# Optimization experiments

Measured on AMD Instinct MI355X. Metric: run time of the kernel, lower is better.

The kernel has to match this reference:

```python
import jax, jax.numpy as jnp
import numpy as np

B, S, HID = 2, 2048, 2048
NH, NKV = 16, 4
HD = HID // NH  # 128
GROUPS = NH // NKV


def _rope(x, cos, sin):
    # x: [B, S, H, D]; cos/sin: [S, D//2]
    xr = x.reshape(*x.shape[:-1], HD // 2, 2)
    x0, x1 = xr[..., 0], xr[..., 1]
    c = cos[None, :, None, :]
    s = sin[None, :, None, :]
    o0 = x0 * c - x1 * s
    o1 = x0 * s + x1 * c
    return jnp.stack([o0, o1], axis=-1).reshape(*x.shape)


def setup_inputs() -> dict:
    key = jax.random.key(0)
    k1, k2, k3, k4, k5, k6 = jax.random.split(key, 6)
    hidden_states = jax.random.normal(k1, (B, S, HID), dtype=jnp.float32)
    # RoPE frequencies (llama-style)
    inv_freq = 1.0 / (10000.0 ** (np.arange(0, HD, 2, dtype=np.float32) / HD))
    t = np.arange(S, dtype=np.float32)
    ang = np.outer(t, inv_freq)  # [S, HD//2]
    freqs_cos = jnp.asarray(np.cos(ang), dtype=jnp.float32)
    freqs_sin = jnp.asarray(np.sin(ang), dtype=jnp.float32)
    # additive causal mask [1,1,S,S]
    causal = jnp.triu(jnp.full((S, S), -1e9, dtype=jnp.float32), k=1)
    attention_mask = causal[None, None]
    sc = 0.02
    Wq = jax.random.normal(k2, (NH * HD, HID), dtype=jnp.float32) * sc
    Wk = jax.random.normal(k3, (NKV * HD, HID), dtype=jnp.float32) * sc
    Wv = jax.random.normal(k4, (NKV * HD, HID), dtype=jnp.float32) * sc
    Wo = jax.random.normal(k5, (HID, NH * HD), dtype=jnp.float32) * sc
    return {"hidden_states": hidden_states, "freqs_cos": freqs_cos,
            "freqs_sin": freqs_sin, "attention_mask": attention_mask,
            "Wq": Wq, "Wk": Wk, "Wv": Wv, "Wo": Wo}


def reference(hidden_states, freqs_cos, freqs_sin, attention_mask, Wq, Wk, Wv, Wo):
    xq = (hidden_states @ Wq.T).reshape(B, S, NH, HD)
    xk = (hidden_states @ Wk.T).reshape(B, S, NKV, HD)
    xv = (hidden_states @ Wv.T).reshape(B, S, NKV, HD)
    xq = _rope(xq, freqs_cos, freqs_sin)
    xk = _rope(xk, freqs_cos, freqs_sin)
    # expand KV heads for GQA: [B,S,NKV,D] -> [B,S,NH,D]
    xk = jnp.repeat(xk, GROUPS, axis=2)
    xv = jnp.repeat(xv, GROUPS, axis=2)
    q = xq.transpose(0, 2, 1, 3)  # [B,H,S,D]
    k = xk.transpose(0, 2, 1, 3)
    v = xv.transpose(0, 2, 1, 3)
    scores = jnp.einsum('bhqd,bhkd->bhqk', q, k) / jnp.sqrt(jnp.float32(HD))
    scores = scores + attention_mask
    probs = jax.nn.softmax(scores, axis=-1)
    out = jnp.einsum('bhqk,bhkd->bhqd', probs, v)
    out = out.transpose(0, 2, 1, 3).reshape(B, S, NH * HD)
    return out @ Wo.T
```

## Files before the change

### kernel.cpp

```cpp
#include <hip/hip_runtime.h>


typedef __attribute__((ext_vector_type(8))) short bf16x8;
typedef __attribute__((ext_vector_type(4))) float f32x4;
typedef __attribute__((ext_vector_type(16))) float f32x16;
typedef __attribute__((ext_vector_type(4))) unsigned short u16x4;
typedef unsigned short u16;

#define B_   2
#define S_   2048
#define HID_ 2048
#define NH_  16
#define NKV_ 4
#define HD_  128

__device__ __forceinline__ u16 f2bf(float f) {
  unsigned u = __float_as_uint(f);
  u = (u + 0x7FFFu + ((u >> 16) & 1u)) >> 16;
  return (u16)u;
}
__device__ __forceinline__ float bf2f(u16 h) {
  return __uint_as_float(((unsigned)h) << 16);
}

__device__ __forceinline__ void gl_lds16(const void* g, void* l) {
  __builtin_amdgcn_global_load_lds(
      (const __attribute__((address_space(1))) void*)g,
      (__attribute__((address_space(3))) void*)l, 16, 0, 0);
}

__global__ void convert_bf16(const float* __restrict__ src, u16* __restrict__ dst, int n8) {
  int i = blockIdx.x * 256 + threadIdx.x;
  if (i >= n8) return;
  const float4* s = (const float4*)src + (size_t)i * 2;
  float4 a = s[0], b = s[1];
  union { u16 u[8]; uint4 v; } o;
  o.u[0] = f2bf(a.x); o.u[1] = f2bf(a.y); o.u[2] = f2bf(a.z); o.u[3] = f2bf(a.w);
  o.u[4] = f2bf(b.x); o.u[5] = f2bf(b.y); o.u[6] = f2bf(b.z); o.u[7] = f2bf(b.w);
  ((uint4*)dst)[i] = o.v;
}

template<int EPI>
__launch_bounds__(256, 2)
__global__ void gemm128(const u16* __restrict__ A, const u16* __restrict__ Bm,
                        float* __restrict__ C, u16* __restrict__ Qb,
                        u16* __restrict__ Kb, u16* __restrict__ Vb,
                        int N, int K)
{
  __shared__ u16 As[128 * 64];
  __shared__ u16 Bs[128 * 64];
  const int tid = threadIdx.x;
  const int lane = tid & 63;
  const int w = tid >> 6;
  const int lo = lane & 15, hi = lane >> 4;
  const int wr = w >> 1, wc = w & 1;
  const int rowA0 = blockIdx.x * 128;
  const int rowB0 = blockIdx.y * 128;

  f32x4 acc[4][4] = {};

  for (int kt = 0; kt < K; kt += 64) {
    __syncthreads();
#pragma unroll
    for (int it = 0; it < 4; ++it) {
      int c = it * 256 + tid;
      int r = c >> 3;
      int cb = (c & 7) * 8;
      gl_lds16(A + (size_t)(rowA0 + r) * K + kt + cb, (char*)As + c * 16);
      gl_lds16(Bm + (size_t)(rowB0 + r) * K + kt + cb, (char*)Bs + c * 16);
    }
    __syncthreads();
#pragma unroll
    for (int kk = 0; kk < 64; kk += 32) {
      bf16x8 af[4], bfr[4];
#pragma unroll
      for (int m = 0; m < 4; ++m)
        af[m] = *(const bf16x8*)(As + (wr * 64 + m * 16 + lo) * 64 + kk + hi * 8);
#pragma unroll
      for (int n = 0; n < 4; ++n)
        bfr[n] = *(const bf16x8*)(Bs + (wc * 64 + n * 16 + lo) * 64 + kk + hi * 8);
#pragma unroll
      for (int m = 0; m < 4; ++m)
#pragma unroll
        for (int n = 0; n < 4; ++n)
          acc[m][n] = __builtin_amdgcn_mfma_f32_16x16x32_bf16(af[m], bfr[n], acc[m][n], 0, 0, 0);
    }
  }

#pragma unroll
  for (int m = 0; m < 4; ++m) {
#pragma unroll
    for (int n = 0; n < 4; ++n) {
#pragma unroll
      for (int r = 0; r < 4; ++r) {
        int grow = rowA0 + wr * 64 + m * 16 + hi * 4 + r;
        int gcol = rowB0 + wc * 64 + n * 16 + lo;
        float v = acc[m][n][r];
        if (EPI == 0) {
          C[(size_t)grow * N + gcol] = v;
        } else {
          int bb = grow >> 11, s = grow & 2047;
          u16 hv = f2bf(v);
          if (gcol < 2048) {
            int h = gcol >> 7, d = gcol & 127;
            Qb[(((size_t)bb * NH_ + h) * S_ + s) * HD_ + d] = hv;
          } else if (gcol < 2560) {
            int h = (gcol - 2048) >> 7, d = gcol & 127;
            Kb[(((size_t)bb * NKV_ + h) * S_ + s) * HD_ + d] = hv;
          } else {
            int h = (gcol - 2560) >> 7, d = gcol & 127;
            Vb[(((size_t)bb * NKV_ + h) * S_ + s) * HD_ + d] = hv;
          }
        }
      }
    }
  }
}

__global__ void rope_k(u16* __restrict__ Qb, u16* __restrict__ Kb,
                       const float* __restrict__ fcos, const float* __restrict__ fsin)
{
  int idx = blockIdx.x * 256 + threadIdx.x;
  int chunk = idx & 15;
  int s = (idx >> 4) & 2047;
  int hs = idx >> 15;
  u16* p = (hs < 32) ? (Qb + ((size_t)hs * S_ + s) * HD_ + chunk * 8)
                     : (Kb + ((size_t)(hs - 32) * S_ + s) * HD_ + chunk * 8);
  uint4 raw = *(uint4*)p;
  float4 c4 = *(const float4*)(fcos + (size_t)s * 64 + chunk * 4);
  float4 s4 = *(const float4*)(fsin + (size_t)s * 64 + chunk * 4);
  float cc[4] = {c4.x, c4.y, c4.z, c4.w};
  float ss[4] = {s4.x, s4.y, s4.z, s4.w};
  unsigned* rw = (unsigned*)&raw;
#pragma unroll
  for (int j = 0; j < 4; ++j) {
    float x0 = bf2f((u16)(rw[j] & 0xFFFFu));
    float x1 = bf2f((u16)(rw[j] >> 16));
    float o0 = x0 * cc[j] - x1 * ss[j];
    float o1 = x0 * ss[j] + x1 * cc[j];
    rw[j] = (unsigned)f2bf(o0) | ((unsigned)f2bf(o1) << 16);
  }
  *(uint4*)p = raw;
}

__global__ void transpose_v(const u16* __restrict__ Vb, u16* __restrict__ Vtg)
{
  __shared__ u16 t[64][65];
  const int st = blockIdx.x, dt = blockIdx.y, hs = blockIdx.z;
  const u16* src = Vb + ((size_t)hs * S_ + st * 64) * HD_ + dt * 64;
#pragma unroll
  for (int it = 0; it < 2; ++it) {
    int c = it * 256 + threadIdx.x;
    int r = c >> 3, cb = (c & 7) * 8;
    uint4 v = *(const uint4*)(src + (size_t)r * HD_ + cb);
    u16* u = (u16*)&v;
#pragma unroll
    for (int e = 0; e < 8; ++e) t[r][cb + e] = u[e];
  }
  __syncthreads();
#pragma unroll
  for (int it = 0; it < 2; ++it) {
    int c = it * 256 + threadIdx.x;
    int r2 = c >> 3, cb2 = (c & 7) * 8;
    union { u16 u[8]; uint4 v; } o;
#pragma unroll
    for (int e = 0; e < 8; ++e) o.u[e] = t[cb2 + e][r2];
    *(uint4*)(Vtg + ((size_t)hs * HD_ + dt * 64 + r2) * S_ + st * 64 + cb2) = o.v;
  }
}

__launch_bounds__(256, 2)
__global__ void flash_attn(const u16* __restrict__ Qb, const u16* __restrict__ Kb,
                           const u16* __restrict__ Vtg, u16* __restrict__ AO)
{
  const int tid = threadIdx.x, lane = tid & 63, w = tid >> 6;
  const int ql = lane & 31, hh = lane >> 5;
  const int x = blockIdx.x, h = blockIdx.y, b = blockIdx.z, kvh = h >> 2;
  const u16* Qh = Qb + ((size_t)b * NH_ + h) * S_ * HD_;
  const u16* Kh = Kb + ((size_t)b * NKV_ + kvh) * S_ * HD_;
  const u16* Vh = Vtg + ((size_t)b * NKV_ + kvh) * HD_ * S_;
  const float cf = 0.12752704581383682f;
  const float NEG = -30000.f;

  const int qt = (w == 0) ? x : (w == 1) ? (63 - x) : (w == 2) ? (31 - x) : (32 + x);
  const int q0 = qt * 32;
  const int qg = q0 + ql;
  const int nt = (qt >> 1) + 1;

  bf16x8 qf[8];
#pragma unroll
  for (int s = 0; s < 8; ++s)
    qf[s] = *(const bf16x8*)(Qh + (size_t)qg * HD_ + s * 16 + hh * 8);

  f32x16 o[4] = {};
  float m = NEG, l = 0.f;

  for (int t = 0; t < nt; ++t) {
    const int kt = t * 64;
    const u16* Kt = Kh + (size_t)kt * HD_;

    bf16x8 k0[8], k1[8];
#pragma unroll
    for (int sl = 0; sl < 8; ++sl)
      k0[sl] = *(const bf16x8*)(Kt + (size_t)ql * HD_ + sl * 16 + hh * 8);
#pragma unroll
    for (int sl = 0; sl < 8; ++sl)
      k1[sl] = *(const bf16x8*)(Kt + (size_t)(32 + ql) * HD_ + sl * 16 + hh * 8);
    f32x16 st[2] = {};
    __builtin_amdgcn_s_setprio(1);
#pragma unroll
    for (int sl = 0; sl < 8; ++sl) {
      st[0] = __builtin_amdgcn_mfma_f32_32x32x16_bf16(k0[sl], qf[sl], st[0], 0, 0, 0);
      st[1] = __builtin_amdgcn_mfma_f32_32x32x16_bf16(k1[sl], qf[sl], st[1], 0, 0, 0);
    }
    __builtin_amdgcn_s_setprio(0);

    if (kt + 63 > q0) {
#pragma unroll
      for (int i = 0; i < 2; ++i)
#pragma unroll
        for (int r = 0; r < 16; ++r) {
          int kv = kt + 32 * i + (r & 3) + 8 * (r >> 2) + 4 * hh;
          if (kv > qg) st[i][r] = NEG;
        }
    }

    float mx[8];
#pragma unroll
    for (int r = 0; r < 8; ++r)
      mx[r] = fmaxf(fmaxf(st[0][r], st[0][r + 8]), fmaxf(st[1][r], st[1][r + 8]));
#pragma unroll
    for (int d = 4; d > 0; d >>= 1)
#pragma unroll
      for (int r = 0; r < d; ++r) mx[r] = fmaxf(mx[r], mx[r + d]);
    float tmax = fmaxf(mx[0], __shfl_xor(mx[0], 32));

    if (!__all((tmax - m) * cf <= 8.f)) {
      float mn = fmaxf(m, tmax);
      float rs = __builtin_exp2f((m - mn) * cf);
      m = mn; l *= rs;
#pragma unroll
      for (int dt = 0; dt < 4; ++dt)
#pragma unroll
        for (int r = 0; r < 16; ++r) o[dt][r] *= rs;
    }

    const float mc = m * cf;
#pragma unroll
    for (int i = 0; i < 2; ++i)
#pragma unroll
      for (int r = 0; r < 16; ++r)
        st[i][r] = __builtin_exp2f(__builtin_fmaf(st[i][r], cf, -mc));
    float sm[8];
#pragma unroll
    for (int r = 0; r < 8; ++r)
      sm[r] = (st[0][r] + st[0][r + 8]) + (st[1][r] + st[1][r + 8]);
#pragma unroll
    for (int d = 4; d > 0; d >>= 1)
#pragma unroll
      for (int r = 0; r < d; ++r) sm[r] += sm[r + d];
    l += sm[0] + __shfl_xor(sm[0], 32);

    bf16x8 pb[4];
#pragma unroll
    for (int i = 0; i < 2; ++i)
#pragma unroll
      for (int s = 0; s < 2; ++s) {
        unsigned wA, wC, wB, wD;
        asm("v_cvt_pk_bf16_f32 %0, %1, %2" : "=v"(wA) : "v"(st[i][8*s+0]), "v"(st[i][8*s+1]));
        asm("v_cvt_pk_bf16_f32 %0, %1, %2" : "=v"(wC) : "v"(st[i][8*s+2]), "v"(st[i][8*s+3]));
        asm("v_cvt_pk_bf16_f32 %0, %1, %2" : "=v"(wB) : "v"(st[i][8*s+4]), "v"(st[i][8*s+5]));
        asm("v_cvt_pk_bf16_f32 %0, %1, %2" : "=v"(wD) : "v"(st[i][8*s+6]), "v"(st[i][8*s+7]));
        unsigned tA = (unsigned)__shfl_xor((int)wA, 32);
        unsigned tB = (unsigned)__shfl_xor((int)wB, 32);
        unsigned tC = (unsigned)__shfl_xor((int)wC, 32);
        unsigned tD = (unsigned)__shfl_xor((int)wD, 32);
        union { unsigned u[4]; bf16x8 v; } pk;
        pk.u[0] = hh ? tB : wA;
        pk.u[1] = hh ? tD : wC;
        pk.u[2] = hh ? wB : tA;
        pk.u[3] = hh ? wD : tC;
        pb[2 * i + s] = pk.v;
      }

#pragma unroll
    for (int dt = 0; dt < 4; ++dt) {
      bf16x8 vf[4];
#pragma unroll
      for (int ks = 0; ks < 4; ++ks)
        vf[ks] = *(const bf16x8*)(Vh + (size_t)(32 * dt + ql) * S_ + kt + ks * 16 + hh * 8);
      __builtin_amdgcn_s_setprio(1);
#pragma unroll
      for (int ks = 0; ks < 4; ++ks)
        o[dt] = __builtin_amdgcn_mfma_f32_32x32x16_bf16(vf[ks], pb[ks], o[dt], 0, 0, 0);
      __builtin_amdgcn_s_setprio(0);
    }
  }

  const float inv = 1.f / l;
#pragma unroll
  for (int dt = 0; dt < 4; ++dt)
#pragma unroll
    for (int g = 0; g < 4; ++g) {
      u16x4 pk4;
#pragma unroll
      for (int e = 0; e < 4; ++e) pk4[e] = f2bf(o[dt][4 * g + e] * inv);
      *(u16x4*)(AO + ((size_t)b * S_ + qg) * HID_ + h * HD_ + 32 * dt + 8 * g + 4 * hh) = pk4;
    }
}

extern "C" void kernel_launch(void* const* d_in, const int* in_sizes, int n_in,
                              void* d_out, int out_size, void* d_ws, size_t ws_size,
                              hipStream_t stream)
{
  (void)in_sizes; (void)n_in; (void)out_size; (void)ws_size;
  const float* X  = (const float*)d_in[0];
  const float* fc = (const float*)d_in[1];
  const float* fs = (const float*)d_in[2];
  const float* Wq = (const float*)d_in[4];
  const float* Wk = (const float*)d_in[5];
  const float* Wv = (const float*)d_in[6];
  const float* Wo = (const float*)d_in[7];
  float* out = (float*)d_out;

  u16* Xb  = (u16*)d_ws;
  u16* Wb  = Xb + (size_t)4096 * 2048;
  u16* Qb  = Wb + (size_t)3072 * 2048;
  u16* Kb  = Qb + (size_t)B_ * NH_ * S_ * HD_;
  u16* Vb  = Kb + (size_t)B_ * NKV_ * S_ * HD_;
  u16* AO  = Xb;
  u16* Wob = Wb;
  u16* Vtg = Wb + (size_t)2048 * 2048;

  convert_bf16<<<4096, 256, 0, stream>>>(X,  Xb,               4096 * 2048 / 8);
  convert_bf16<<<2048, 256, 0, stream>>>(Wq, Wb,               2048 * 2048 / 8);
  convert_bf16<<<512,  256, 0, stream>>>(Wk, Wb + 2048 * 2048, 512 * 2048 / 8);
  convert_bf16<<<512,  256, 0, stream>>>(Wv, Wb + 2560 * 2048, 512 * 2048 / 8);

  gemm128<1><<<dim3(32, 24), 256, 0, stream>>>(Xb, Wb, nullptr, Qb, Kb, Vb, 3072, 2048);

  convert_bf16<<<2048, 256, 0, stream>>>(Wo, Wob, 2048 * 2048 / 8);

  transpose_v<<<dim3(32, 2, 8), 256, 0, stream>>>(Vb, Vtg);

  rope_k<<<5120, 256, 0, stream>>>(Qb, Kb, fc, fs);

  flash_attn<<<dim3(16, NH_, B_), 256, 0, stream>>>(Qb, Kb, Vtg, AO);

  gemm128<0><<<dim3(32, 16), 256, 0, stream>>>(AO, Wob, out, nullptr, nullptr, nullptr, 2048, 2048);
}
```

Before: 289.8 us.

## Double-buffer K tile loads and prefetch V fragments in flash attention loop

The attention inner loop now keeps two register buffers for K tiles and issues the next tile's K loads right after the current QK^T MFMAs, so global-memory latency overlaps with softmax and PV work. V fragments are split into two halves loaded earlier, before masking and the softmax, so they are in flight during that computation. This raises register pressure considerably (32 extra bf16x8 K registers plus 16 V registers), which may lower occupancy or cause spills.

```diff
diff --git a/kernel.cpp b/kernel.cpp
--- a/kernel.cpp
+++ b/kernel.cpp
@@ -195,25 +195,37 @@
   f32x16 o[4] = {};
   float m = NEG, l = 0.f;
 
-  for (int t = 0; t < nt; ++t) {
+  bf16x8 kA[16], kB[16];
+
+  auto loadK = [&](bf16x8 (&kd)[16], int t) {
+    const u16* Kt = Kh + (size_t)(t * 64) * HD_;
+#pragma unroll
+    for (int sl = 0; sl < 8; ++sl) {
+      kd[sl]     = *(const bf16x8*)(Kt + (size_t)ql * HD_ + sl * 16 + hh * 8);
+      kd[8 + sl] = *(const bf16x8*)(Kt + (size_t)(32 + ql) * HD_ + sl * 16 + hh * 8);
+    }
+  };
+
+  auto body = [&](bf16x8 (&kc)[16], bf16x8 (&kn)[16], int t) {
     const int kt = t * 64;
-    const u16* Kt = Kh + (size_t)kt * HD_;
-
-    bf16x8 k0[8], k1[8];
-#pragma unroll
-    for (int sl = 0; sl < 8; ++sl)
-      k0[sl] = *(const bf16x8*)(Kt + (size_t)ql * HD_ + sl * 16 + hh * 8);
-#pragma unroll
-    for (int sl = 0; sl < 8; ++sl)
-      k1[sl] = *(const bf16x8*)(Kt + (size_t)(32 + ql) * HD_ + sl * 16 + hh * 8);
+
     f32x16 st[2] = {};
     __builtin_amdgcn_s_setprio(1);
 #pragma unroll
     for (int sl = 0; sl < 8; ++sl) {
-      st[0] = __builtin_amdgcn_mfma_f32_32x32x16_bf16(k0[sl], qf[sl], st[0], 0, 0, 0);
-      st[1] = __builtin_amdgcn_mfma_f32_32x32x16_bf16(k1[sl], qf[sl], st[1], 0, 0, 0);
+      st[0] = __builtin_amdgcn_mfma_f32_32x32x16_bf16(kc[sl],     qf[sl], st[0], 0, 0, 0);
+      st[1] = __builtin_amdgcn_mfma_f32_32x32x16_bf16(kc[8 + sl], qf[sl], st[1], 0, 0, 0);
     }
     __builtin_amdgcn_s_setprio(0);
+
+    if (t + 1 < nt) loadK(kn, t + 1);
+
+    bf16x8 vf0[8];
+#pragma unroll
+    for (int dt = 0; dt < 2; ++dt)
+#pragma unroll
+      for (int ks = 0; ks < 4; ++ks)
+        vf0[4 * dt + ks] = *(const bf16x8*)(Vh + (size_t)(32 * dt + ql) * S_ + kt + ks * 16 + hh * 8);
 
     if (kt + 63 > q0) {
 #pragma unroll
@@ -283,18 +295,31 @@
         pb[2 * i + s] = pk.v;
       }
 
-#pragma unroll
-    for (int dt = 0; dt < 4; ++dt) {
-      bf16x8 vf[4];
+    bf16x8 vf1[8];
+#pragma unroll
+    for (int dt = 0; dt < 2; ++dt)
 #pragma unroll
       for (int ks = 0; ks < 4; ++ks)
-        vf[ks] = *(const bf16x8*)(Vh + (size_t)(32 * dt + ql) * S_ + kt + ks * 16 + hh * 8);
-      __builtin_amdgcn_s_setprio(1);
+        vf1[4 * dt + ks] = *(const bf16x8*)(Vh + (size_t)(64 + 32 * dt + ql) * S_ + kt + ks * 16 + hh * 8);
+
+    __builtin_amdgcn_s_setprio(1);
+#pragma unroll
+    for (int dt = 0; dt < 2; ++dt)
 #pragma unroll
       for (int ks = 0; ks < 4; ++ks)
-        o[dt] = __builtin_amdgcn_mfma_f32_32x32x16_bf16(vf[ks], pb[ks], o[dt], 0, 0, 0);
-      __builtin_amdgcn_s_setprio(0);
-    }
+        o[dt] = __builtin_amdgcn_mfma_f32_32x32x16_bf16(vf0[4 * dt + ks], pb[ks], o[dt], 0, 0, 0);
+#pragma unroll
+    for (int dt = 0; dt < 2; ++dt)
+#pragma unroll
+      for (int ks = 0; ks < 4; ++ks)
+        o[2 + dt] = __builtin_amdgcn_mfma_f32_32x32x16_bf16(vf1[4 * dt + ks], pb[ks], o[2 + dt], 0, 0, 0);
+    __builtin_amdgcn_s_setprio(0);
+  };
+
+  loadK(kA, 0);
+  for (int t = 0; t < nt; ++t) {
+    if (t & 1) body(kB, kA, t);
+    else       body(kA, kB, t);
   }
 
   const float inv = 1.f / l;
```

New measurement: 648.5 us. 124% more time.

## Rework flash attention to 16x16x32 MFMA tiles with LDS P-reshuffle

Applied to the files above, without the earlier changes.

The flash attention kernel now uses 16-row query tiles per wave with 16x16x32 bf16 MFMAs instead of 32-row tiles with 32x32x16. The P matrix goes through a small per-wave LDS buffer instead of cross-lane shuffles. The grid becomes 1024 blocks with a linearised index that groups blocks sharing a KV head for cache locality. Launch bounds rise to 4 blocks per SM for higher occupancy. In exchange, each K and V element is reloaded for twice as many query tiles, and LDS traffic is added for P.

```diff
diff --git a/kernel.cpp b/kernel.cpp
--- a/kernel.cpp
+++ b/kernel.cpp
@@ -3,7 +3,6 @@
 
 typedef __attribute__((ext_vector_type(8))) short bf16x8;
 typedef __attribute__((ext_vector_type(4))) float f32x4;
-typedef __attribute__((ext_vector_type(16))) float f32x16;
 typedef __attribute__((ext_vector_type(4))) unsigned short u16x4;
 typedef unsigned short u16;
 
@@ -169,144 +168,145 @@
   }
 }
 
-__launch_bounds__(256, 2)
+__launch_bounds__(256, 4)
 __global__ void flash_attn(const u16* __restrict__ Qb, const u16* __restrict__ Kb,
                            const u16* __restrict__ Vtg, u16* __restrict__ AO)
 {
+  __shared__ u16 Ps[4][16 * 72];
+
   const int tid = threadIdx.x, lane = tid & 63, w = tid >> 6;
-  const int ql = lane & 31, hh = lane >> 5;
-  const int x = blockIdx.x, h = blockIdx.y, b = blockIdx.z, kvh = h >> 2;
+  const int qi = lane & 15, lh = lane >> 4;
+  const int lin = blockIdx.x;
+  const int g = lin & 7, idx = lin >> 3;
+  const int b = g >> 2, kvh = g & 3;
+  const int h = kvh * 4 + (idx >> 5);
+  const int x = idx & 31;
+
   const u16* Qh = Qb + ((size_t)b * NH_ + h) * S_ * HD_;
   const u16* Kh = Kb + ((size_t)b * NKV_ + kvh) * S_ * HD_;
   const u16* Vh = Vtg + ((size_t)b * NKV_ + kvh) * HD_ * S_;
   const float cf = 0.12752704581383682f;
   const float NEG = -30000.f;
 
-  const int qt = (w == 0) ? x : (w == 1) ? (63 - x) : (w == 2) ? (31 - x) : (32 + x);
-  const int q0 = qt * 32;
-  const int qg = q0 + ql;
-  const int nt = (qt >> 1) + 1;
-
-  bf16x8 qf[8];
-#pragma unroll
-  for (int s = 0; s < 8; ++s)
-    qf[s] = *(const bf16x8*)(Qh + (size_t)qg * HD_ + s * 16 + hh * 8);
-
-  f32x16 o[4] = {};
+  const int qt = (w == 0) ? x : (w == 1) ? (127 - x) : (w == 2) ? (63 - x) : (64 + x);
+  const int q0 = qt * 16;
+  const int qg = q0 + qi;
+  const int nt = (qt >> 2) + 1;
+
+  bf16x8 qf[4];
+#pragma unroll
+  for (int kc = 0; kc < 4; ++kc)
+    qf[kc] = *(const bf16x8*)(Qh + (size_t)qg * HD_ + kc * 32 + lh * 8);
+
+  f32x4 o[8] = {};
   float m = NEG, l = 0.f;
 
   for (int t = 0; t < nt; ++t) {
     const int kt = t * 64;
     const u16* Kt = Kh + (size_t)kt * HD_;
 
-    bf16x8 k0[8], k1[8];
-#pragma unroll
-    for (int sl = 0; sl < 8; ++sl)
-      k0[sl] = *(const bf16x8*)(Kt + (size_t)ql * HD_ + sl * 16 + hh * 8);
-#pragma unroll
-    for (int sl = 0; sl < 8; ++sl)
-      k1[sl] = *(const bf16x8*)(Kt + (size_t)(32 + ql) * HD_ + sl * 16 + hh * 8);
-    f32x16 st[2] = {};
-    __builtin_amdgcn_s_setprio(1);
-#pragma unroll
-    for (int sl = 0; sl < 8; ++sl) {
-      st[0] = __builtin_amdgcn_mfma_f32_32x32x16_bf16(k0[sl], qf[sl], st[0], 0, 0, 0);
-      st[1] = __builtin_amdgcn_mfma_f32_32x32x16_bf16(k1[sl], qf[sl], st[1], 0, 0, 0);
-    }
-    __builtin_amdgcn_s_setprio(0);
+    f32x4 st[4] = {};
+#pragma unroll
+    for (int gp = 0; gp < 2; ++gp) {
+      bf16x8 k0[4], k1[4];
+#pragma unroll
+      for (int kc = 0; kc < 4; ++kc) {
+        k0[kc] = *(const bf16x8*)(Kt + (size_t)(32 * gp + qi) * HD_ + kc * 32 + lh * 8);
+        k1[kc] = *(const bf16x8*)(Kt + (size_t)(32 * gp + 16 + qi) * HD_ + kc * 32 + lh * 8);
+      }
+      __builtin_amdgcn_s_setprio(1);
+#pragma unroll
+      for (int kc = 0; kc < 4; ++kc) {
+        st[2 * gp]     = __builtin_amdgcn_mfma_f32_16x16x32_bf16(k0[kc], qf[kc], st[2 * gp], 0, 0, 0);
+        st[2 * gp + 1] = __builtin_amdgcn_mfma_f32_16x16x32_bf16(k1[kc], qf[kc], st[2 * gp + 1], 0, 0, 0);
+      }
+      __builtin_amdgcn_s_setprio(0);
+    }
 
     if (kt + 63 > q0) {
 #pragma unroll
-      for (int i = 0; i < 2; ++i)
-#pragma unroll
-        for (int r = 0; r < 16; ++r) {
-          int kv = kt + 32 * i + (r & 3) + 8 * (r >> 2) + 4 * hh;
-          if (kv > qg) st[i][r] = NEG;
+      for (int gg = 0; gg < 4; ++gg)
+#pragma unroll
+        for (int r = 0; r < 4; ++r) {
+          int kv = kt + 16 * gg + 4 * lh + r;
+          if (kv > qg) st[gg][r] = NEG;
         }
     }
 
-    float mx[8];
-#pragma unroll
-    for (int r = 0; r < 8; ++r)
-      mx[r] = fmaxf(fmaxf(st[0][r], st[0][r + 8]), fmaxf(st[1][r], st[1][r + 8]));
-#pragma unroll
-    for (int d = 4; d > 0; d >>= 1)
-#pragma unroll
-      for (int r = 0; r < d; ++r) mx[r] = fmaxf(mx[r], mx[r + d]);
-    float tmax = fmaxf(mx[0], __shfl_xor(mx[0], 32));
-
-    if (!__all((tmax - m) * cf <= 8.f)) {
-      float mn = fmaxf(m, tmax);
+    float mx = st[0][0];
+#pragma unroll
+    for (int gg = 0; gg < 4; ++gg)
+#pragma unroll
+      for (int r = 0; r < 4; ++r) mx = fmaxf(mx, st[gg][r]);
+    mx = fmaxf(mx, __shfl_xor(mx, 16));
+    mx = fmaxf(mx, __shfl_xor(mx, 32));
+
+    if (!__all((mx - m) * cf <= 8.f)) {
+      float mn = fmaxf(m, mx);
       float rs = __builtin_exp2f((m - mn) * cf);
       m = mn; l *= rs;
 #pragma unroll
-      for (int dt = 0; dt < 4; ++dt)
-#pragma unroll
-        for (int r = 0; r < 16; ++r) o[dt][r] *= rs;
+      for (int dg = 0; dg < 8; ++dg)
+#pragma unroll
+        for (int r = 0; r < 4; ++r) o[dg][r] *= rs;
     }
 
     const float mc = m * cf;
 #pragma unroll
-    for (int i = 0; i < 2; ++i)
-#pragma unroll
-      for (int r = 0; r < 16; ++r)
-        st[i][r] = __builtin_exp2f(__builtin_fmaf(st[i][r], cf, -mc));
-    float sm[8];
-#pragma unroll
-    for (int r = 0; r < 8; ++r)
-      sm[r] = (st[0][r] + st[0][r + 8]) + (st[1][r] + st[1][r + 8]);
-#pragma unroll
-    for (int d = 4; d > 0; d >>= 1)
-#pragma unroll
-      for (int r = 0; r < d; ++r) sm[r] += sm[r + d];
-    l += sm[0] + __shfl_xor(sm[0], 32);
-
-    bf16x8 pb[4];
-#pragma unroll
-    for (int i = 0; i < 2; ++i)
-#pragma unroll
-      for (int s = 0; s < 2; ++s) {
-        unsigned wA, wC, wB, wD;
-        asm("v_cvt_pk_bf16_f32 %0, %1, %2" : "=v"(wA) : "v"(st[i][8*s+0]), "v"(st[i][8*s+1]));
-        asm("v_cvt_pk_bf16_f32 %0, %1, %2" : "=v"(wC) : "v"(st[i][8*s+2]), "v"(st[i][8*s+3]));
-        asm("v_cvt_pk_bf16_f32 %0, %1, %2" : "=v"(wB) : "v"(st[i][8*s+4]), "v"(st[i][8*s+5]));
-        asm("v_cvt_pk_bf16_f32 %0, %1, %2" : "=v"(wD) : "v"(st[i][8*s+6]), "v"(st[i][8*s+7]));
-        unsigned tA = (unsigned)__shfl_xor((int)wA, 32);
-        unsigned tB = (unsigned)__shfl_xor((int)wB, 32);
-        unsigned tC = (unsigned)__shfl_xor((int)wC, 32);
-        unsigned tD = (unsigned)__shfl_xor((int)wD, 32);
-        union { unsigned u[4]; bf16x8 v; } pk;
-        pk.u[0] = hh ? tB : wA;
-        pk.u[1] = hh ? tD : wC;
-        pk.u[2] = hh ? wB : tA;
-        pk.u[3] = hh ? wD : tC;
-        pb[2 * i + s] = pk.v;
-      }
-
-#pragma unroll
-    for (int dt = 0; dt < 4; ++dt) {
-      bf16x8 vf[4];
-#pragma unroll
-      for (int ks = 0; ks < 4; ++ks)
-        vf[ks] = *(const bf16x8*)(Vh + (size_t)(32 * dt + ql) * S_ + kt + ks * 16 + hh * 8);
+    for (int gg = 0; gg < 4; ++gg)
+#pragma unroll
+      for (int r = 0; r < 4; ++r)
+        st[gg][r] = __builtin_exp2f(__builtin_fmaf(st[gg][r], cf, -mc));
+    float s = 0.f;
+#pragma unroll
+    for (int gg = 0; gg < 4; ++gg)
+      s += (st[gg][0] + st[gg][1]) + (st[gg][2] + st[gg][3]);
+    s += __shfl_xor(s, 16);
+    s += __shfl_xor(s, 32);
+    l += s;
+
+    unsigned pkw[8];
+#pragma unroll
+    for (int gg = 0; gg < 4; ++gg) {
+      asm("v_cvt_pk_bf16_f32 %0, %1, %2" : "=v"(pkw[2 * gg])     : "v"(st[gg][0]), "v"(st[gg][1]));
+      asm("v_cvt_pk_bf16_f32 %0, %1, %2" : "=v"(pkw[2 * gg + 1]) : "v"(st[gg][2]), "v"(st[gg][3]));
+    }
+#pragma unroll
+    for (int gg = 0; gg < 4; ++gg) {
+      uint2 wv; wv.x = pkw[2 * gg]; wv.y = pkw[2 * gg + 1];
+      *(uint2*)(&Ps[w][qi * 72 + 16 * gg + 4 * lh]) = wv;
+    }
+    bf16x8 pb[2];
+#pragma unroll
+    for (int kc2 = 0; kc2 < 2; ++kc2)
+      pb[kc2] = *(const bf16x8*)(&Ps[w][qi * 72 + kc2 * 32 + lh * 8]);
+
+#pragma unroll
+    for (int dp = 0; dp < 4; ++dp) {
+      bf16x8 v0[2], v1[2];
+#pragma unroll
+      for (int kc2 = 0; kc2 < 2; ++kc2) {
+        v0[kc2] = *(const bf16x8*)(Vh + (size_t)(32 * dp + qi) * S_ + kt + kc2 * 32 + lh * 8);
+        v1[kc2] = *(const bf16x8*)(Vh + (size_t)(32 * dp + 16 + qi) * S_ + kt + kc2 * 32 + lh * 8);
+      }
       __builtin_amdgcn_s_setprio(1);
 #pragma unroll
-      for (int ks = 0; ks < 4; ++ks)
-        o[dt] = __builtin_amdgcn_mfma_f32_32x32x16_bf16(vf[ks], pb[ks], o[dt], 0, 0, 0);
+      for (int kc2 = 0; kc2 < 2; ++kc2) {
+        o[2 * dp]     = __builtin_amdgcn_mfma_f32_16x16x32_bf16(v0[kc2], pb[kc2], o[2 * dp], 0, 0, 0);
+        o[2 * dp + 1] = __builtin_amdgcn_mfma_f32_16x16x32_bf16(v1[kc2], pb[kc2], o[2 * dp + 1], 0, 0, 0);
+      }
       __builtin_amdgcn_s_setprio(0);
     }
   }
 
   const float inv = 1.f / l;
 #pragma unroll
-  for (int dt = 0; dt < 4; ++dt)
-#pragma unroll
-    for (int g = 0; g < 4; ++g) {
-      u16x4 pk4;
-#pragma unroll
-      for (int e = 0; e < 4; ++e) pk4[e] = f2bf(o[dt][4 * g + e] * inv);
-      *(u16x4*)(AO + ((size_t)b * S_ + qg) * HID_ + h * HD_ + 32 * dt + 8 * g + 4 * hh) = pk4;
-    }
+  for (int dg = 0; dg < 8; ++dg) {
+    u16x4 pk4;
+#pragma unroll
+    for (int r = 0; r < 4; ++r) pk4[r] = f2bf(o[dg][r] * inv);
+    *(u16x4*)(AO + ((size_t)b * S_ + qg) * HID_ + h * HD_ + 16 * dg + 4 * lh) = pk4;
+  }
 }
 
 extern "C" void kernel_launch(void* const* d_in, const int* in_sizes, int n_in,
@@ -345,7 +345,7 @@
 
   rope_k<<<5120, 256, 0, stream>>>(Qb, Kb, fc, fs);
 
-  flash_attn<<<dim3(16, NH_, B_), 256, 0, stream>>>(Qb, Kb, Vtg, AO);
+  flash_attn<<<1024, 256, 0, stream>>>(Qb, Kb, Vtg, AO);
 
   gemm128<0><<<dim3(32, 16), 256, 0, stream>>>(AO, Wob, out, nullptr, nullptr, nullptr, 2048, 2048);
 }
```

Result: slower. 385.2 us (+32.9%).
